# Kernel tuning notes

Measured on AMD Instinct MI355X. Metric: run time of the kernel, lower is better.

The kernel has to match this reference:

```python
import jax, jax.numpy as jnp
import numpy as np

FILTERS = 128
STRIDE = 4
CHANNEL_MULTIPLIER = 2
N_EVENTS = 4194304
N_OUT = 65536


def setup_inputs() -> dict:
    key = jax.random.key(0)
    k1, k2, k3, k4, k5 = jax.random.split(key, 5)
    dt = jax.random.uniform(k1, (N_EVENTS,), dtype=jnp.float32)  # nonneg time deltas
    times_out = jnp.sort(jax.random.uniform(k2, (N_OUT,), dtype=jnp.float32))
    successor_kernel_channel_ids = jax.random.randint(
        k3, (N_EVENTS,), 0, STRIDE * FILTERS, dtype=jnp.int32)
    segment_ids_out = jax.random.randint(k4, (N_EVENTS,), 0, N_OUT, dtype=jnp.int32)
    # learned parameter: pre-activation decay rate, shape (filters, channel_multiplier)
    decay_rate = jax.random.normal(k5, (FILTERS, CHANNEL_MULTIPLIER), dtype=jnp.float32) * 0.1
    return {
        "dt": dt,
        "times_out": times_out,
        "decay_rate": decay_rate,
        "successor_kernel_channel_ids": successor_kernel_channel_ids,
        "segment_ids_out": segment_ids_out,
    }


def reference(dt, times_out, decay_rate, successor_kernel_channel_ids, segment_ids_out):
    # softplus activation on the raw decay_rate parameter (decay_rate_activation='softplus')
    rate = jax.nn.softplus(decay_rate)  # [F, M]
    F, M = rate.shape
    n_out = times_out.shape[0]
    # decode channel from the combined (kernel, channel) id: id = kernel * F + channel
    channel = successor_kernel_channel_ids % F  # [E]
    # per-event decayed one-hot value: exp(-rate[channel] * dt), shape [E, M]
    vals = jnp.exp(-rate[channel] * dt[:, None])
    # exclusive scatter-add into slot (segment, kernel*F + channel)
    flat_ids = segment_ids_out * (STRIDE * F) + successor_kernel_channel_ids  # [E]
    pooled = jax.ops.segment_sum(vals, flat_ids, num_segments=n_out * STRIDE * F,
                                 indices_are_sorted=False)  # [n_out*S*F, M]
    return pooled.reshape(n_out, STRIDE * F * M)
```

## Files before the change

### kernel.cpp

```cpp
#include <hip/hip_runtime.h>
#include <hip/hip_bf16.h>


#define F 128
#define M 2
#define SF 512
#define ROW 1024
#define NFINE 4096
#define NC 256
#define SEGS_PER_BIN 16
#define NBLK 256
#define CAPC 20480
#define CAPF 1280
#define CHUNK 8192

typedef float vfloat4 __attribute__((ext_vector_type(4)));

__global__ void __launch_bounds__(256)
init_cursors(unsigned* __restrict__ gcur) {
    gcur[threadIdx.x] = (unsigned)threadIdx.x * CAPC;
}

__global__ void __launch_bounds__(1024)
p3a_fused(const float* __restrict__ dt, const int* __restrict__ kc,
          const int* __restrict__ seg, unsigned* __restrict__ gcur,
          unsigned* __restrict__ rec2, int epb) {
    __shared__ int      hist[NC];
    __shared__ unsigned cur[NC];
    size_t base = (size_t)blockIdx.x * epb;
    int nchunks = epb / CHUNK;

    for (int ck = 0; ck < nchunks; ck++) {
        if (threadIdx.x < NC) hist[threadIdx.x] = 0;
        __syncthreads();

        size_t cb0 = base + (size_t)ck * CHUNK + (size_t)threadIdx.x * 4;
        size_t cb1 = cb0 + (CHUNK / 2);
        uint4  s0 = *(const uint4*)((const unsigned*)seg + cb0);
        uint4  s1 = *(const uint4*)((const unsigned*)seg + cb1);
        uint4  k0 = *(const uint4*)((const unsigned*)kc + cb0);
        uint4  k1 = *(const uint4*)((const unsigned*)kc + cb1);
        float4 d0 = *(const float4*)(dt + cb0);
        float4 d1 = *(const float4*)(dt + cb1);

        atomicAdd(&hist[s0.x >> 8], 1);
        atomicAdd(&hist[s0.y >> 8], 1);
        atomicAdd(&hist[s0.z >> 8], 1);
        atomicAdd(&hist[s0.w >> 8], 1);
        atomicAdd(&hist[s1.x >> 8], 1);
        atomicAdd(&hist[s1.y >> 8], 1);
        atomicAdd(&hist[s1.z >> 8], 1);
        atomicAdd(&hist[s1.w >> 8], 1);
        __syncthreads();

        if (threadIdx.x < NC) {
            int h = hist[threadIdx.x];
            if (h > 0)
                cur[threadIdx.x] = atomicAdd(&gcur[threadIdx.x], (unsigned)h);
        }
        __syncthreads();

#define EMIT(S, K, D)                                                        \
        {                                                                    \
            unsigned q = min(32767u, (unsigned)((D) * 32768.0f));            \
            unsigned pos = atomicAdd(&cur[(S) >> 8], 1u);                    \
            rec2[pos] = (q << 17) | (((S) & 255u) << 9) | (K);               \
        }
        EMIT(s0.x, k0.x, d0.x) EMIT(s0.y, k0.y, d0.y)
        EMIT(s0.z, k0.z, d0.z) EMIT(s0.w, k0.w, d0.w)
        EMIT(s1.x, k1.x, d1.x) EMIT(s1.y, k1.y, d1.y)
        EMIT(s1.z, k1.z, d1.z) EMIT(s1.w, k1.w, d1.w)
#undef EMIT
        __syncthreads();
    }
}

__global__ void __launch_bounds__(1024)
p3b_scatter(const unsigned* __restrict__ rec2,
            const unsigned* __restrict__ gcur,
            unsigned* __restrict__ rec, unsigned* __restrict__ fend) {
    __shared__ unsigned cur[16];
    unsigned c = blockIdx.x;
    unsigned start = c * CAPC;
    unsigned end   = gcur[c];
    unsigned cnt   = end - start;
    unsigned n4    = cnt >> 2;
    if (threadIdx.x < 16)
        cur[threadIdx.x] = (c * 16u + threadIdx.x) * CAPF;
    __syncthreads();

#define ROUTE(V)                                                             \
    {                                                                        \
        unsigned pos = atomicAdd(&cur[((V) >> 13) & 15u], 1u);               \
        rec[pos] = (V);                                                      \
    }
    const uint4* q4 = (const uint4*)(rec2 + start);
    for (unsigned i = threadIdx.x; i < n4; i += 1024) {
        uint4 v = q4[i];
        ROUTE(v.x) ROUTE(v.y) ROUTE(v.z) ROUTE(v.w)
    }
    for (unsigned r = start + (n4 << 2) + threadIdx.x; r < end; r += 1024)
        ROUTE(rec2[r])
#undef ROUTE
    __syncthreads();
    if (threadIdx.x < 16)
        fend[c * 16u + threadIdx.x] = cur[threadIdx.x];
}

__global__ void __launch_bounds__(512)
p4_accum(const unsigned* __restrict__ rec, const unsigned* __restrict__ fend,
         const float* __restrict__ decay, float* __restrict__ out) {
    __shared__ float acc[SEGS_PER_BIN * ROW];
    __shared__ float rl2[F * M];
    if (threadIdx.x < F * M) {
        float x = decay[threadIdx.x];
        float sp = fmaxf(x, 0.0f) + log1pf(expf(-fabsf(x)));
        rl2[threadIdx.x] = -sp * (1.4426950408889634f / 32768.0f);
    }
    vfloat4* a4 = (vfloat4*)acc;
    for (int i = threadIdx.x; i < SEGS_PER_BIN * ROW / 4; i += 512)
        a4[i] = (vfloat4)0.0f;
    __syncthreads();

    unsigned b = blockIdx.x;
    unsigned start = b * CAPF;
    unsigned end   = fend[b];
    unsigned cnt   = end - start;
    unsigned n2    = cnt >> 1;

#define PROC(V)                                                              \
    {                                                                        \
        unsigned id = (V) & 511u;                                            \
        unsigned ls = ((V) >> 9) & 15u;                                      \
        float    t  = (float)((V) >> 17) + 0.5f;                             \
        unsigned ch = id & (F - 1);                                          \
        unsigned bs = ls * ROW + id * M;                                     \
        atomicAdd(&acc[bs + 0], exp2f(rl2[ch * M + 0] * t));                 \
        atomicAdd(&acc[bs + 1], exp2f(rl2[ch * M + 1] * t));                 \
    }
    const uint2* q2 = (const uint2*)(rec + start);
    for (unsigned i = threadIdx.x; i < n2; i += 512) {
        uint2 v = q2[i];
        PROC(v.x) PROC(v.y)
    }
    if ((cnt & 1u) && threadIdx.x == 0)
        PROC(rec[end - 1])
#undef PROC
    __syncthreads();

    vfloat4* o4 = (vfloat4*)(out + (size_t)b * (SEGS_PER_BIN * ROW));
    for (int i = threadIdx.x; i < SEGS_PER_BIN * ROW / 4; i += 512)
        __builtin_nontemporal_store(a4[i], &o4[i]);
}

__global__ void __launch_bounds__(256)
zero_fill_kernel(float4* __restrict__ out, size_t n4) {
    size_t stride = (size_t)gridDim.x * blockDim.x;
    const float4 z = make_float4(0.f, 0.f, 0.f, 0.f);
    for (size_t i = (size_t)blockIdx.x * blockDim.x + threadIdx.x; i < n4; i += stride)
        out[i] = z;
}

__global__ void __launch_bounds__(256)
onehot_scatter_kernel(const float* __restrict__ dt,
                      const float* __restrict__ decay_rate,
                      const int* __restrict__ kc_ids,
                      const int* __restrict__ seg_ids,
                      float* __restrict__ out,
                      int n_events) {
    __shared__ float rate[F * M];
    for (int i = threadIdx.x; i < F * M; i += blockDim.x) {
        float x = decay_rate[i];
        rate[i] = fmaxf(x, 0.0f) + log1pf(expf(-fabsf(x)));
    }
    __syncthreads();
    int stride = gridDim.x * blockDim.x;
    for (int e = blockIdx.x * blockDim.x + threadIdx.x; e < n_events; e += stride) {
        float d  = dt[e];
        int   id = kc_ids[e];
        int   sg = seg_ids[e];
        int   ch = id & (F - 1);
        size_t o = ((size_t)sg * SF + (size_t)id) * M;
        atomicAdd(&out[o + 0], expf(-rate[ch * M + 0] * d));
        atomicAdd(&out[o + 1], expf(-rate[ch * M + 1] * d));
    }
}

extern "C" void kernel_launch(void* const* d_in, const int* in_sizes, int n_in,
                              void* d_out, int out_size, void* d_ws, size_t ws_size,
                              hipStream_t stream) {
    const float* dt         = (const float*)d_in[0];
    const float* decay_rate = (const float*)d_in[2];
    const int*   kc_ids     = (const int*)d_in[3];
    const int*   seg_ids    = (const int*)d_in[4];
    float*       out        = (float*)d_out;

    int n_events = in_sizes[0];
    int n_out    = in_sizes[1];

    size_t slabc_bytes = (size_t)NC * CAPC * sizeof(unsigned);
    size_t slabf_bytes = (size_t)NFINE * CAPF * sizeof(unsigned);
    size_t need = slabc_bytes + slabf_bytes + (NC + NFINE) * sizeof(unsigned);

    bool shapes_ok = (n_out == 65536) &&
                     ((size_t)out_size == (size_t)n_out * ROW) &&
                     (ws_size >= need) &&
                     (n_events == 4 * 1024 * 1024);

    if (!shapes_ok) {
        zero_fill_kernel<<<4096, 256, 0, stream>>>((float4*)out,
                                                   (size_t)out_size / 4);
        int grid = (n_events + 255) / 256;
        onehot_scatter_kernel<<<grid, 256, 0, stream>>>(
            dt, decay_rate, kc_ids, seg_ids, out, n_events);
        return;
    }

    char* p = (char*)d_ws;
    unsigned* rec2 = (unsigned*)p;  p += slabc_bytes;
    unsigned* rec  = (unsigned*)p;  p += slabf_bytes;
    unsigned* gcur = (unsigned*)p;  p += NC * sizeof(unsigned);
    unsigned* fend = (unsigned*)p;

    int epb = n_events / NBLK;

    init_cursors<<<1, 256, 0, stream>>>(gcur);
    p3a_fused<<<NBLK, 1024, 0, stream>>>(dt, kc_ids, seg_ids, gcur, rec2, epb);
    p3b_scatter<<<NC, 1024, 0, stream>>>(rec2, gcur, rec, fend);
    p4_accum<<<NFINE, 512, 0, stream>>>(rec, fend, decay_rate, out);
}
```

Before: 374.7 us.

## Drop fine scatter pass; filter coarse slab per sub-bin in accumulate kernel

Removes the second scatter kernel that routed records into fine bins. Instead, each accumulate block reads the entire coarse bin's record slab and processes only the records matching its sub-bin. Blocks are remapped so all sub-bins of a coarse bin land on the same XCD to share L2. This trades a kernel launch plus a global write/read of all records for 16x redundant reads of each coarse slab, which are likely served from L2.

```diff
diff --git a/kernel.cpp b/kernel.cpp
--- a/kernel.cpp
+++ b/kernel.cpp
@@ -11,7 +11,6 @@
 #define SEGS_PER_BIN 16
 #define NBLK 256
 #define CAPC 20480
-#define CAPF 1280
 #define CHUNK 8192
 
 typedef float vfloat4 __attribute__((ext_vector_type(4)));
@@ -75,40 +74,8 @@
     }
 }
 
-__global__ void __launch_bounds__(1024)
-p3b_scatter(const unsigned* __restrict__ rec2,
-            const unsigned* __restrict__ gcur,
-            unsigned* __restrict__ rec, unsigned* __restrict__ fend) {
-    __shared__ unsigned cur[16];
-    unsigned c = blockIdx.x;
-    unsigned start = c * CAPC;
-    unsigned end   = gcur[c];
-    unsigned cnt   = end - start;
-    unsigned n4    = cnt >> 2;
-    if (threadIdx.x < 16)
-        cur[threadIdx.x] = (c * 16u + threadIdx.x) * CAPF;
-    __syncthreads();
-
-#define ROUTE(V)                                                             \
-    {                                                                        \
-        unsigned pos = atomicAdd(&cur[((V) >> 13) & 15u], 1u);               \
-        rec[pos] = (V);                                                      \
-    }
-    const uint4* q4 = (const uint4*)(rec2 + start);
-    for (unsigned i = threadIdx.x; i < n4; i += 1024) {
-        uint4 v = q4[i];
-        ROUTE(v.x) ROUTE(v.y) ROUTE(v.z) ROUTE(v.w)
-    }
-    for (unsigned r = start + (n4 << 2) + threadIdx.x; r < end; r += 1024)
-        ROUTE(rec2[r])
-#undef ROUTE
-    __syncthreads();
-    if (threadIdx.x < 16)
-        fend[c * 16u + threadIdx.x] = cur[threadIdx.x];
-}
-
 __global__ void __launch_bounds__(512)
-p4_accum(const unsigned* __restrict__ rec, const unsigned* __restrict__ fend,
+p4_accum(const unsigned* __restrict__ rec2, const unsigned* __restrict__ gcur,
          const float* __restrict__ decay, float* __restrict__ out) {
     __shared__ float acc[SEGS_PER_BIN * ROW];
     __shared__ float rl2[F * M];
@@ -122,11 +89,17 @@
         a4[i] = (vfloat4)0.0f;
     __syncthreads();
 
-    unsigned b = blockIdx.x;
-    unsigned start = b * CAPF;
-    unsigned end   = fend[b];
+    unsigned b   = blockIdx.x;
+    unsigned xcd = b & 7u;
+    unsigned idx = b >> 3;
+    unsigned c   = xcd * 32u + (idx >> 4);
+    unsigned sub = idx & 15u;
+    unsigned fb  = c * 16u + sub;
+
+    unsigned start = c * CAPC;
+    unsigned end   = gcur[c];
     unsigned cnt   = end - start;
-    unsigned n2    = cnt >> 1;
+    unsigned n4    = cnt >> 2;
 
 #define PROC(V)                                                              \
     {                                                                        \
@@ -138,17 +111,22 @@
         atomicAdd(&acc[bs + 0], exp2f(rl2[ch * M + 0] * t));                 \
         atomicAdd(&acc[bs + 1], exp2f(rl2[ch * M + 1] * t));                 \
     }
-    const uint2* q2 = (const uint2*)(rec + start);
-    for (unsigned i = threadIdx.x; i < n2; i += 512) {
-        uint2 v = q2[i];
-        PROC(v.x) PROC(v.y)
-    }
-    if ((cnt & 1u) && threadIdx.x == 0)
-        PROC(rec[end - 1])
+    const uint4* q4 = (const uint4*)(rec2 + start);
+    for (unsigned i = threadIdx.x; i < n4; i += 512) {
+        uint4 v = q4[i];
+        if (((v.x >> 13) & 15u) == sub) PROC(v.x)
+        if (((v.y >> 13) & 15u) == sub) PROC(v.y)
+        if (((v.z >> 13) & 15u) == sub) PROC(v.z)
+        if (((v.w >> 13) & 15u) == sub) PROC(v.w)
+    }
+    for (unsigned r = start + (n4 << 2) + threadIdx.x; r < end; r += 512) {
+        unsigned v = rec2[r];
+        if (((v >> 13) & 15u) == sub) PROC(v)
+    }
 #undef PROC
     __syncthreads();
 
-    vfloat4* o4 = (vfloat4*)(out + (size_t)b * (SEGS_PER_BIN * ROW));
+    vfloat4* o4 = (vfloat4*)(out + (size_t)fb * (SEGS_PER_BIN * ROW));
     for (int i = threadIdx.x; i < SEGS_PER_BIN * ROW / 4; i += 512)
         __builtin_nontemporal_store(a4[i], &o4[i]);
 }
@@ -199,8 +177,7 @@
     int n_out    = in_sizes[1];
 
     size_t slabc_bytes = (size_t)NC * CAPC * sizeof(unsigned);
-    size_t slabf_bytes = (size_t)NFINE * CAPF * sizeof(unsigned);
-    size_t need = slabc_bytes + slabf_bytes + (NC + NFINE) * sizeof(unsigned);
+    size_t need = slabc_bytes + NC * sizeof(unsigned);
 
     bool shapes_ok = (n_out == 65536) &&
                      ((size_t)out_size == (size_t)n_out * ROW) &&
@@ -218,14 +195,11 @@
 
     char* p = (char*)d_ws;
     unsigned* rec2 = (unsigned*)p;  p += slabc_bytes;
-    unsigned* rec  = (unsigned*)p;  p += slabf_bytes;
-    unsigned* gcur = (unsigned*)p;  p += NC * sizeof(unsigned);
-    unsigned* fend = (unsigned*)p;
+    unsigned* gcur = (unsigned*)p;
 
     int epb = n_events / NBLK;
 
     init_cursors<<<1, 256, 0, stream>>>(gcur);
     p3a_fused<<<NBLK, 1024, 0, stream>>>(dt, kc_ids, seg_ids, gcur, rec2, epb);
-    p3b_scatter<<<NC, 1024, 0, stream>>>(rec2, gcur, rec, fend);
-    p4_accum<<<NFINE, 512, 0, stream>>>(rec, fend, decay_rate, out);
-}
+    p4_accum<<<NFINE, 512, 0, stream>>>(rec2, gcur, decay_rate, out);
+}
```

After: 373.8 us. No clear change (-0.2%).
